# Kernel optimization log

Hardware: AMD Instinct MI355X
Metric: run time of the kernel (lower is better)

Reference implementation:

```python
import jax, jax.numpy as jnp
import numpy as np

N = 100000
E = 1600000
D_IN = 128
D_HID = 128
D_OUT = 64
NUM_LAYERS = 4


def setup_inputs() -> dict:
    key = jax.random.key(0)
    ks = jax.random.split(key, 12)
    features = jax.random.normal(ks[0], (N, D_IN), dtype=jnp.float32)
    edge_index = jax.random.randint(ks[1], (2, E), 0, N, dtype=jnp.int64)
    def glorot(k, shape):
        fan_in, fan_out = shape
        s = jnp.sqrt(6.0 / (fan_in + fan_out)).astype(jnp.float32)
        return jax.random.uniform(k, shape, jnp.float32, -s, s)
    W0 = glorot(ks[2], (D_IN, D_HID)); b0 = jnp.zeros((D_HID,), jnp.float32)
    W1 = glorot(ks[3], (D_HID, D_HID)); b1 = jnp.zeros((D_HID,), jnp.float32)
    W2 = glorot(ks[4], (D_HID, D_HID)); b2 = jnp.zeros((D_HID,), jnp.float32)
    W3 = glorot(ks[5], (D_HID, D_OUT)); b3 = jnp.zeros((D_OUT,), jnp.float32)
    return {"features": features, "edge_index": edge_index,
            "W0": W0, "b0": b0, "W1": W1, "b1": b1,
            "W2": W2, "b2": b2, "W3": W3, "b3": b3}


def _degree_norms(edge_index):
    src, dst = edge_index[0], edge_index[1]
    ones = jnp.ones((src.shape[0],), jnp.float32)
    out_deg = jax.ops.segment_sum(ones, src, num_segments=N)
    in_deg = jax.ops.segment_sum(ones, dst, num_segments=N)
    norm_src = jnp.where(out_deg > 0, jax.lax.rsqrt(jnp.maximum(out_deg, 1.0)), 0.0)
    norm_dst = jnp.where(in_deg > 0, jax.lax.rsqrt(jnp.maximum(in_deg, 1.0)), 0.0)
    return norm_src, norm_dst


def _graph_conv(x, W, b, src, dst, norm_src, norm_dst, act):
    # linear transform first (aggregation is linear, order-equivalent)
    h = x @ W                                   # [N, d_out]
    h = h * norm_src[:, None]                   # symmetric norm, src side
    msg = jnp.take(h, src, axis=0)              # gather  [E, d_out]
    agg = jax.ops.segment_sum(msg, dst, num_segments=N)  # scatter-add [N, d_out]
    agg = agg * norm_dst[:, None]               # symmetric norm, dst side
    agg = agg + b
    if act:
        agg = jnp.tanh(agg)
    return agg


def reference(features, edge_index, W0, b0, W1, b1, W2, b2, W3, b3):
    src, dst = edge_index[0], edge_index[1]
    norm_src, norm_dst = _degree_norms(edge_index)
    x = _graph_conv(features, W0, b0, src, dst, norm_src, norm_dst, act=True)
    x = _graph_conv(x, W1, b1, src, dst, norm_src, norm_dst, act=True)
    x = _graph_conv(x, W2, b2, src, dst, norm_src, norm_dst, act=True)
    x = _graph_conv(x, W3, b3, src, dst, norm_src, norm_dst, act=False)  # last layer: no activation
    return x
```

## Files before the change

kernel.cpp:

```cpp
#include <hip/hip_runtime.h>
#include <cmath>

typedef __attribute__((ext_vector_type(8))) short bf16x8;
typedef __attribute__((ext_vector_type(8))) _Float16 f16x8;
typedef __attribute__((ext_vector_type(4))) float f32x4;

__device__ inline unsigned short f2bf_rne(float f) {
    unsigned int u = __float_as_uint(f);
    unsigned int r = (u + 0x7FFFu + ((u >> 16) & 1u)) >> 16;
    return (unsigned short)r;
}
__device__ inline float bf2f(unsigned short h) {
    return __uint_as_float(((unsigned int)h) << 16);
}

__device__ inline float fast_tanh(float x) {
    float e = x * 2.8853900817779268f;
    e = fminf(fmaxf(e, -126.f), 126.f);
    float t = __builtin_amdgcn_exp2f(e);
    return (t - 1.0f) * __builtin_amdgcn_rcpf(t + 1.0f);
}


constexpr int CB = 256;

__global__ __launch_bounds__(256) void k_bucket_hist(const int* __restrict__ src,
                                                     const int* __restrict__ dst,
                                                     int* __restrict__ gH,
                                                     int E, int K, int scanN, int chunk) {
    extern __shared__ int lds[];
    int* hd = lds; int* hs = lds + K;
    for (int i = threadIdx.x; i < 2 * K; i += 256) lds[i] = 0;
    __syncthreads();
    int lo = blockIdx.x * chunk;
    int hi = lo + chunk; if (hi > E) hi = E;
    for (int i = lo + threadIdx.x; i < hi; i += 256) {
        atomicAdd(&hd[dst[i] >> 6], 1);
        atomicAdd(&hs[src[i] >> 6], 1);
    }
    __syncthreads();
    for (int k = threadIdx.x; k < K; k += 256) {
        gH[(size_t)k * CB + blockIdx.x] = hd[k];
        gH[(size_t)(scanN + k * CB) + blockIdx.x] = hs[k];
    }
}

__global__ __launch_bounds__(256) void k_bucket_scatter(const int* __restrict__ src,
                                                        const int* __restrict__ dst,
                                                        const int* __restrict__ gHS,
                                                        int* __restrict__ sortedAll,
                                                        int E, int K, int scanN, int chunk) {
    extern __shared__ int lds[];
    int* bd = lds; int* bs = lds + K;
    for (int k = threadIdx.x; k < K; k += 256) {
        bd[k] = gHS[(size_t)k * CB + blockIdx.x];
        bs[k] = gHS[(size_t)(scanN + k * CB) + blockIdx.x];
    }
    __syncthreads();
    int lo = blockIdx.x * chunk;
    int hi = lo + chunk; if (hi > E) hi = E;
    for (int i = lo + threadIdx.x; i < hi; i += 256) {
        int d = dst[i], s = src[i];
        int pd = atomicAdd(&bd[d >> 6], 1);
        sortedAll[pd] = ((d & 63) << 17) | s;
        int ps = atomicAdd(&bs[s >> 6], 1);
        sortedAll[ps] = s;
    }
}

__global__ __launch_bounds__(256) void k_fine(const int* __restrict__ sortedAll,
                                              const int* __restrict__ gHS,
                                              int* __restrict__ rowptr,
                                              int* __restrict__ colidx,
                                              float* __restrict__ nsrc,
                                              float* __restrict__ ndst,
                                              int E, int K, int scanN, int N) {
    __shared__ int cnt[64], excl[64], rank[64];
    int kb = blockIdx.x;
    bool isDst = kb < K;
    int k = isDst ? kb : kb - K;
    int bstart, bend;
    if (isDst) {
        bstart = gHS[(size_t)k * CB];
        bend = (k + 1 < K) ? gHS[(size_t)(k + 1) * CB] : E;
    } else {
        bstart = gHS[(size_t)(scanN + k * CB)];
        bend = (k + 1 < K) ? gHS[(size_t)(scanN + (k + 1) * CB)] : 2 * E;
    }
    if (threadIdx.x < 64) { cnt[threadIdx.x] = 0; rank[threadIdx.x] = 0; }
    __syncthreads();
    if (isDst) {
        for (int i = bstart + threadIdx.x; i < bend; i += 256)
            atomicAdd(&cnt[sortedAll[i] >> 17], 1);
    } else {
        for (int i = bstart + threadIdx.x; i < bend; i += 256)
            atomicAdd(&cnt[sortedAll[i] & 63], 1);
    }
    __syncthreads();
    if (isDst) {
        if (threadIdx.x == 0) {
            int r = 0;
            for (int j = 0; j < 64; j++) { excl[j] = r; r += cnt[j]; }
        }
        __syncthreads();
        int node0 = k << 6;
        if (threadIdx.x < 64) {
            int node = node0 + threadIdx.x;
            if (node < N) {
                rowptr[node] = bstart + excl[threadIdx.x];
                int c = cnt[threadIdx.x];
                ndst[node] = c > 0 ? rsqrtf((float)c) : 0.f;
            }
        }
        if (k == 0 && threadIdx.x == 0) rowptr[N] = E;
        for (int i = bstart + threadIdx.x; i < bend; i += 256) {
            int v = sortedAll[i];
            int n = v >> 17;
            int r = atomicAdd(&rank[n], 1);
            colidx[bstart + excl[n] + r] = v & 0x1FFFF;
        }
    } else {
        int node = (k << 6) + threadIdx.x;
        if (threadIdx.x < 64 && node < N) {
            int c = cnt[threadIdx.x];
            nsrc[node] = c > 0 ? rsqrtf((float)c) : 0.f;
        }
    }
}

__global__ void k_prepW_all(const float* __restrict__ W0, const float* __restrict__ W1,
                            const float* __restrict__ W2, const float* __restrict__ W3,
                            unsigned short* __restrict__ h0, unsigned short* __restrict__ l0,
                            unsigned short* __restrict__ h1, unsigned short* __restrict__ l1,
                            unsigned short* __restrict__ h2, unsigned short* __restrict__ l2,
                            unsigned short* __restrict__ h3, unsigned short* __restrict__ l3) {
    int i = blockIdx.x * 256 + threadIdx.x;
    const float* W; unsigned short* wh; unsigned short* wl; int N; int base; bool bf;
    if      (i < 16384) { W = W0; wh = h0; wl = l0; N = 128; base = i;         bf = true;  }
    else if (i < 32768) { W = W1; wh = h1; wl = l1; N = 128; base = i - 16384; bf = false; }
    else if (i < 49152) { W = W2; wh = h2; wl = l2; N = 128; base = i - 32768; bf = false; }
    else if (i < 57344) { W = W3; wh = h3; wl = l3; N = 64;  base = i - 49152; bf = false; }
    else return;
    int n = base >> 7, k = base & 127;
    float w = W[k * N + n];
    if (bf) {
        unsigned short hb = f2bf_rne(w);
        unsigned short lb = f2bf_rne(w - bf2f(hb));
        wh[base] = hb; wl[base] = lb;
    } else {
        union { _Float16 f; unsigned short u; } H, L;
        H.f = (_Float16)w;
        L.f = (_Float16)(w - (float)H.f);
        wh[base] = H.u; wl[base] = L.u;
    }
}


constexpr int SCAN_TILE = 2048;

__global__ __launch_bounds__(256) void k_scan_partial(const int* __restrict__ deg,
                                                      int* __restrict__ tilesum, int n) {
    __shared__ int red[256];
    int base = blockIdx.x * SCAN_TILE;
    int s = 0;
    for (int i = threadIdx.x; i < SCAN_TILE; i += 256) {
        int idx = base + i;
        if (idx < n) s += deg[idx];
    }
    red[threadIdx.x] = s;
    __syncthreads();
    for (int off = 128; off > 0; off >>= 1) {
        if (threadIdx.x < off) red[threadIdx.x] += red[threadIdx.x + off];
        __syncthreads();
    }
    if (threadIdx.x == 0) tilesum[blockIdx.x] = red[0];
}

__global__ void k_scan_tiles(int* __restrict__ tilesum, int* __restrict__ outArr,
                             int numTiles, int n) {
    if (threadIdx.x == 0 && blockIdx.x == 0) {
        int acc = 0;
        for (int i = 0; i < numTiles; i++) { int v = tilesum[i]; tilesum[i] = acc; acc += v; }
        outArr[n] = acc;
    }
}

__global__ __launch_bounds__(256) void k_scan_final(const int* __restrict__ deg,
                                                    const int* __restrict__ tilesum,
                                                    int* __restrict__ outArr, int n) {
    __shared__ int red[256];
    int base = blockIdx.x * SCAN_TILE;
    int lo = base + threadIdx.x * 8;
    int v[8]; int s = 0;
#pragma unroll
    for (int j = 0; j < 8; j++) {
        int idx = lo + j;
        v[j] = (idx < n) ? deg[idx] : 0;
        s += v[j];
    }
    red[threadIdx.x] = s;
    __syncthreads();
    for (int off = 1; off < 256; off <<= 1) {
        int x = red[threadIdx.x];
        int add = (threadIdx.x >= off) ? red[threadIdx.x - off] : 0;
        __syncthreads();
        red[threadIdx.x] = x + add;
        __syncthreads();
    }
    int excl = tilesum[blockIdx.x] + (threadIdx.x ? red[threadIdx.x - 1] : 0);
#pragma unroll
    for (int j = 0; j < 8; j++) {
        int idx = lo + j;
        if (idx < n) outArr[idx] = excl;
        excl += v[j];
    }
}


template <int DOUT, int SRC>
__global__ __launch_bounds__(256) void k_gemm_hyb(
        const float* __restrict__ xf, const _Float16* __restrict__ xq,
        const unsigned short* __restrict__ wth, const unsigned short* __restrict__ wtl,
        const float* __restrict__ nsrc, _Float16* __restrict__ h, int nrows) {
    constexpr int NT = DOUT / 16;
    constexpr int LDK = 72;
    __shared__ unsigned short Bh[DOUT * LDK], Bl[DOUT * LDK];

    int tid = threadIdx.x;
    int lane = tid & 63;
    int wv = tid >> 6;
    int quad = lane >> 4, l16 = lane & 15;
    int r0 = blockIdx.x * 64 + wv * 16;
    int rowA = r0 + l16; if (rowA >= nrows) rowA = nrows - 1;

    if (blockIdx.x == 0 && tid < DOUT / 8) {
        float4 z = {0.f, 0.f, 0.f, 0.f};
        *(float4*)((char*)h + ((size_t)nrows * DOUT + tid * 8) * 2) = z;
    }

    f32x4 acc[NT];
#pragma unroll
    for (int nt = 0; nt < NT; nt++) acc[nt] = (f32x4){0.f, 0.f, 0.f, 0.f};

    for (int kh = 0; kh < 2; kh++) {
        if (kh) __syncthreads();
        for (int i = tid; i < DOUT * 16; i += 256) {
            int n = i >> 4, kb = i & 15;
            int koff = kh * 64 + kb * 4;
            *(ushort4*)&Bh[n * LDK + kb * 4] = *(const ushort4*)&wth[n * 128 + koff];
            *(ushort4*)&Bl[n * LDK + kb * 4] = *(const ushort4*)&wtl[n * 128 + koff];
        }
        __syncthreads();

#pragma unroll
        for (int kq = 0; kq < 2; kq++) {
            int koA = kh * 64 + kq * 32 + quad * 8;
            int koB = kq * 32 + quad * 8;
            if (SRC == 0) {
                const float* xp = &xf[(size_t)rowA * 128 + koA];
                float4 x0 = *(const float4*)xp;
                float4 x1 = *(const float4*)(xp + 4);
                union { bf16x8 v; unsigned short u[8]; } H, L;
                float xs[8] = {x0.x, x0.y, x0.z, x0.w, x1.x, x1.y, x1.z, x1.w};
#pragma unroll
                for (int j = 0; j < 8; j++) {
                    H.u[j] = f2bf_rne(xs[j]);
                    L.u[j] = f2bf_rne(xs[j] - bf2f(H.u[j]));
                }
                bf16x8 ah = H.v, al = L.v;
#pragma unroll
                for (int nt = 0; nt < NT; nt++) {
                    int n = nt * 16 + l16;
                    bf16x8 bh = *(const bf16x8*)&Bh[n * LDK + koB];
                    bf16x8 bl = *(const bf16x8*)&Bl[n * LDK + koB];
                    acc[nt] = __builtin_amdgcn_mfma_f32_16x16x32_bf16(ah, bh, acc[nt], 0, 0, 0);
                    acc[nt] = __builtin_amdgcn_mfma_f32_16x16x32_bf16(ah, bl, acc[nt], 0, 0, 0);
                    acc[nt] = __builtin_amdgcn_mfma_f32_16x16x32_bf16(al, bh, acc[nt], 0, 0, 0);
                }
            } else {
                f16x8 aq = *(const f16x8*)&xq[(size_t)rowA * 128 + koA];
#pragma unroll
                for (int nt = 0; nt < NT; nt++) {
                    int n = nt * 16 + l16;
                    f16x8 bh = *(const f16x8*)&Bh[n * LDK + koB];
                    f16x8 bl = *(const f16x8*)&Bl[n * LDK + koB];
                    acc[nt] = __builtin_amdgcn_mfma_f32_16x16x32_f16(aq, bh, acc[nt], 0, 0, 0);
                    acc[nt] = __builtin_amdgcn_mfma_f32_16x16x32_f16(aq, bl, acc[nt], 0, 0, 0);
                }
            }
        }
    }

#pragma unroll
    for (int r = 0; r < 4; r++) {
        int row = r0 + quad * 4 + r;
        if (row < nrows) {
            float nm = nsrc[row];
#pragma unroll
            for (int nt = 0; nt < NT; nt++)
                h[(size_t)row * DOUT + nt * 16 + l16] = (_Float16)(acc[nt][r] * nm);
        }
    }
}


template <int D, int MODE>
__global__ __launch_bounds__(256) void k_aggregate(const _Float16* __restrict__ h,
                                                   const int* __restrict__ rowptr,
                                                   const int* __restrict__ colidx,
                                                   const float* __restrict__ ndst,
                                                   const float* __restrict__ bias,
                                                   float* __restrict__ out,
                                                   _Float16* __restrict__ oq,
                                                   int n) {
    constexpr int FB = D / 8;
    constexpr int GN = 64 / FB;
    constexpr int EU = 4;
    int wid  = (blockIdx.x * 256 + threadIdx.x) >> 6;
    int lane = threadIdx.x & 63;
    int fb = lane & (FB - 1);
    int g  = lane / FB;
    int waveCount = gridDim.x * 4;

    for (int nbase = wid * GN; nbase < n; nbase += waveCount * GN) {
        int node = nbase + g;
        bool vn = node < n;
        int beg = vn ? rowptr[node] : 0;
        int end = vn ? rowptr[node + 1] : 0;
        int m = end - beg;

        int mmax = m;
#pragma unroll
        for (int off = FB; off < 64; off <<= 1) {
            int t = __shfl_xor(mmax, off);
            mmax = mmax > t ? mmax : t;
        }

        float acc[8];
#pragma unroll
        for (int k = 0; k < 8; k++) acc[k] = 0.f;

        int cv = 0;
        for (int j0 = 0; j0 < mmax; j0 += EU) {
            if ((j0 & (FB - 1)) == 0) {
                int idx = beg + j0 + fb;
                cv = __builtin_nontemporal_load(&colidx[idx < end ? idx : 0]);
            }
            int s[EU];
#pragma unroll
            for (int u = 0; u < EU; u++) {
                int j = j0 + u;
                int sv = __shfl(cv, g * FB + (j & (FB - 1)));
                s[u] = j < m ? sv : n;
            }
            f16x8 v[EU];
#pragma unroll
            for (int u = 0; u < EU; u++)
                v[u] = *(const f16x8*)&h[(size_t)s[u] * D + fb * 8];
#pragma unroll
            for (int u = 0; u < EU; u++) {
#pragma unroll
                for (int k = 0; k < 8; k++)
                    acc[k] += (float)v[u][k];
            }
        }

        if (vn) {
            float nd = ndst[node];
            float bv[8];
            *(float4*)&bv[0] = ((const float4*)bias)[fb * 2];
            *(float4*)&bv[4] = ((const float4*)bias)[fb * 2 + 1];
            float vv[8];
#pragma unroll
            for (int k = 0; k < 8; k++) vv[k] = acc[k] * nd + bv[k];
            if (MODE == 1) {
                f16x8 q;
#pragma unroll
                for (int k = 0; k < 8; k++)
                    q[k] = (_Float16)fast_tanh(vv[k]);
                *(f16x8*)&oq[(size_t)node * D + fb * 8] = q;
            } else {
                *(float4*)&out[(size_t)node * D + fb * 8] = *(float4*)&vv[0];
                *(float4*)&out[(size_t)node * D + fb * 8 + 4] = *(float4*)&vv[4];
            }
        }
    }
}


extern "C" void kernel_launch(void* const* d_in, const int* in_sizes, int n_in,
                              void* d_out, int out_size, void* d_ws, size_t ws_size,
                              hipStream_t stream) {
    const float* features = (const float*)d_in[0];
    const int* edges      = (const int*)d_in[1];
    const float* W0 = (const float*)d_in[2]; const float* b0 = (const float*)d_in[3];
    const float* W1 = (const float*)d_in[4]; const float* b1 = (const float*)d_in[5];
    const float* W2 = (const float*)d_in[6]; const float* b2 = (const float*)d_in[7];
    const float* W3 = (const float*)d_in[8]; const float* b3 = (const float*)d_in[9];
    float* out = (float*)d_out;

    const int N = in_sizes[0] / 128;
    const int E = in_sizes[1] / 2;
    const int* src = edges;
    const int* dst = edges + E;
    const int K = (N + 63) >> 6;
    const int chunk = (E + CB - 1) / CB;
    const int scanN = K * CB;
    const int n2 = 2 * scanN;
    const int numTiles = (n2 + SCAN_TILE - 1) / SCAN_TILE;
    const size_t dynLds = (size_t)2 * K * sizeof(int);

    char* p = (char*)d_ws;
    _Float16* bufH         = (_Float16*)p;       p += (size_t)N * 128 * 4;
    _Float16* xq           = (_Float16*)p;       p += (size_t)(N + 1) * 128 * 2;
    char*     xspare       = p;                  p += (size_t)(N + 1) * 128 * 2;
    int*   rowptr = (int*)p;   p += (((size_t)(N + 1) * 4 + 15) / 16) * 16;
    int*   colidx = (int*)p;   p += (size_t)E * 4;
    float* nsrc   = (float*)p; p += (size_t)N * 4;
    float* ndst   = (float*)p; p += (size_t)N * 4;
    int*   tilesum= (int*)p;   p += (((size_t)(numTiles + 1) * 4 + 15) / 16) * 16;
    unsigned short* wt0h = (unsigned short*)p; p += 16384 * 2;
    unsigned short* wt0l = (unsigned short*)p; p += 16384 * 2;
    unsigned short* wt1h = (unsigned short*)p; p += 16384 * 2;
    unsigned short* wt1l = (unsigned short*)p; p += 16384 * 2;
    unsigned short* wt2h = (unsigned short*)p; p += 16384 * 2;
    unsigned short* wt2l = (unsigned short*)p; p += 16384 * 2;
    unsigned short* wt3h = (unsigned short*)p; p += 8192 * 2;
    unsigned short* wt3l = (unsigned short*)p; p += 8192 * 2;

    char* q = (char*)xq;
    int* sortedAll = (int*)q; q += (size_t)2 * E * 4;
    int* gH        = (int*)q; q += (size_t)n2 * 4;
    int* gHS       = (int*)q; q += (size_t)(n2 + 1) * 4;
    (void)xspare;

    k_prepW_all<<<224, 256, 0, stream>>>(W0, W1, W2, W3, wt0h, wt0l, wt1h, wt1l,
                                         wt2h, wt2l, wt3h, wt3l);
    k_bucket_hist<<<CB, 256, dynLds, stream>>>(src, dst, gH, E, K, scanN, chunk);
    k_scan_partial<<<numTiles, 256, 0, stream>>>(gH, tilesum, n2);
    k_scan_tiles<<<1, 64, 0, stream>>>(tilesum, gHS, numTiles, n2);
    k_scan_final<<<numTiles, 256, 0, stream>>>(gH, tilesum, gHS, n2);
    k_bucket_scatter<<<CB, 256, dynLds, stream>>>(src, dst, gHS, sortedAll, E, K, scanN, chunk);
    k_fine<<<2 * K, 256, 0, stream>>>(sortedAll, gHS, rowptr, colidx, nsrc, ndst, E, K, scanN, N);

    int gblk = (N + 63) / 64;
    int ablk128 = (N + 15) / 16;
    int ablk64  = (N + 31) / 32;
    k_gemm_hyb<128, 0><<<gblk, 256, 0, stream>>>(features, nullptr, wt0h, wt0l, nsrc, bufH, N);
    k_aggregate<128, 1><<<ablk128, 256, 0, stream>>>(bufH, rowptr, colidx, ndst, b0, nullptr, xq, N);
    k_gemm_hyb<128, 1><<<gblk, 256, 0, stream>>>(nullptr, xq, wt1h, wt1l, nsrc, bufH, N);
    k_aggregate<128, 1><<<ablk128, 256, 0, stream>>>(bufH, rowptr, colidx, ndst, b1, nullptr, xq, N);
    k_gemm_hyb<128, 1><<<gblk, 256, 0, stream>>>(nullptr, xq, wt2h, wt2l, nsrc, bufH, N);
    k_aggregate<128, 1><<<ablk128, 256, 0, stream>>>(bufH, rowptr, colidx, ndst, b2, nullptr, xq, N);
    k_gemm_hyb<64, 1><<<gblk, 256, 0, stream>>>(nullptr, xq, wt3h, wt3l, nsrc, bufH, N);
    k_aggregate<64, 0><<<ablk64, 256, 0, stream>>>(bufH, rowptr, colidx, ndst, b3, out, nullptr, N);
}
```

Before: 508.9 us.

## Compute out-degree with global atomics and tile multiple row blocks per GEMM wave

Out-degree is now counted with direct global atomics into a per-node array, zeroed in the weight-prep kernel. This drops the second half of the bucket sort, scan and fine pass that previously existed only to obtain source degrees. The GEMM kernel gains an RT template parameter so each wave handles two 16-row tiles, reusing the B fragments loaded from LDS across more MFMAs. Nontemporal loads and stores are added for activations. Global atomics on random source indices may contend, and the larger tiles raise register pressure.

```diff
diff --git a/kernel.cpp b/kernel.cpp
--- a/kernel.cpp
+++ b/kernel.cpp
@@ -27,35 +27,31 @@
 __global__ __launch_bounds__(256) void k_bucket_hist(const int* __restrict__ src,
                                                      const int* __restrict__ dst,
                                                      int* __restrict__ gH,
-                                                     int E, int K, int scanN, int chunk) {
+                                                     int* __restrict__ odeg,
+                                                     int E, int K, int chunk) {
     extern __shared__ int lds[];
-    int* hd = lds; int* hs = lds + K;
-    for (int i = threadIdx.x; i < 2 * K; i += 256) lds[i] = 0;
+    for (int i = threadIdx.x; i < K; i += 256) lds[i] = 0;
     __syncthreads();
     int lo = blockIdx.x * chunk;
     int hi = lo + chunk; if (hi > E) hi = E;
     for (int i = lo + threadIdx.x; i < hi; i += 256) {
-        atomicAdd(&hd[dst[i] >> 6], 1);
-        atomicAdd(&hs[src[i] >> 6], 1);
-    }
-    __syncthreads();
-    for (int k = threadIdx.x; k < K; k += 256) {
-        gH[(size_t)k * CB + blockIdx.x] = hd[k];
-        gH[(size_t)(scanN + k * CB) + blockIdx.x] = hs[k];
-    }
+        atomicAdd(&lds[dst[i] >> 6], 1);
+        atomicAdd(&odeg[src[i]], 1);
+    }
+    __syncthreads();
+    for (int k = threadIdx.x; k < K; k += 256)
+        gH[(size_t)k * CB + blockIdx.x] = lds[k];
 }
 
 __global__ __launch_bounds__(256) void k_bucket_scatter(const int* __restrict__ src,
                                                         const int* __restrict__ dst,
                                                         const int* __restrict__ gHS,
                                                         int* __restrict__ sortedAll,
-                                                        int E, int K, int scanN, int chunk) {
+                                                        int E, int K, int chunk) {
     extern __shared__ int lds[];
-    int* bd = lds; int* bs = lds + K;
-    for (int k = threadIdx.x; k < K; k += 256) {
+    int* bd = lds;
+    for (int k = threadIdx.x; k < K; k += 256)
         bd[k] = gHS[(size_t)k * CB + blockIdx.x];
-        bs[k] = gHS[(size_t)(scanN + k * CB) + blockIdx.x];
-    }
     __syncthreads();
     int lo = blockIdx.x * chunk;
     int hi = lo + chunk; if (hi > E) hi = E;
@@ -63,68 +59,48 @@
         int d = dst[i], s = src[i];
         int pd = atomicAdd(&bd[d >> 6], 1);
         sortedAll[pd] = ((d & 63) << 17) | s;
-        int ps = atomicAdd(&bs[s >> 6], 1);
-        sortedAll[ps] = s;
     }
 }
 
 __global__ __launch_bounds__(256) void k_fine(const int* __restrict__ sortedAll,
                                               const int* __restrict__ gHS,
+                                              const int* __restrict__ odeg,
                                               int* __restrict__ rowptr,
                                               int* __restrict__ colidx,
                                               float* __restrict__ nsrc,
                                               float* __restrict__ ndst,
-                                              int E, int K, int scanN, int N) {
+                                              int E, int K, int N) {
     __shared__ int cnt[64], excl[64], rank[64];
-    int kb = blockIdx.x;
-    bool isDst = kb < K;
-    int k = isDst ? kb : kb - K;
-    int bstart, bend;
-    if (isDst) {
-        bstart = gHS[(size_t)k * CB];
-        bend = (k + 1 < K) ? gHS[(size_t)(k + 1) * CB] : E;
-    } else {
-        bstart = gHS[(size_t)(scanN + k * CB)];
-        bend = (k + 1 < K) ? gHS[(size_t)(scanN + (k + 1) * CB)] : 2 * E;
-    }
+    int k = blockIdx.x;
+    int bstart = gHS[(size_t)k * CB];
+    int bend   = gHS[(size_t)(k + 1) * CB];
     if (threadIdx.x < 64) { cnt[threadIdx.x] = 0; rank[threadIdx.x] = 0; }
     __syncthreads();
-    if (isDst) {
-        for (int i = bstart + threadIdx.x; i < bend; i += 256)
-            atomicAdd(&cnt[sortedAll[i] >> 17], 1);
-    } else {
-        for (int i = bstart + threadIdx.x; i < bend; i += 256)
-            atomicAdd(&cnt[sortedAll[i] & 63], 1);
-    }
-    __syncthreads();
-    if (isDst) {
-        if (threadIdx.x == 0) {
-            int r = 0;
-            for (int j = 0; j < 64; j++) { excl[j] = r; r += cnt[j]; }
-        }
-        __syncthreads();
-        int node0 = k << 6;
-        if (threadIdx.x < 64) {
-            int node = node0 + threadIdx.x;
-            if (node < N) {
-                rowptr[node] = bstart + excl[threadIdx.x];
-                int c = cnt[threadIdx.x];
-                ndst[node] = c > 0 ? rsqrtf((float)c) : 0.f;
-            }
-        }
-        if (k == 0 && threadIdx.x == 0) rowptr[N] = E;
-        for (int i = bstart + threadIdx.x; i < bend; i += 256) {
-            int v = sortedAll[i];
-            int n = v >> 17;
-            int r = atomicAdd(&rank[n], 1);
-            colidx[bstart + excl[n] + r] = v & 0x1FFFF;
-        }
-    } else {
-        int node = (k << 6) + threadIdx.x;
-        if (threadIdx.x < 64 && node < N) {
+    for (int i = bstart + threadIdx.x; i < bend; i += 256)
+        atomicAdd(&cnt[sortedAll[i] >> 17], 1);
+    __syncthreads();
+    if (threadIdx.x == 0) {
+        int r = 0;
+        for (int j = 0; j < 64; j++) { excl[j] = r; r += cnt[j]; }
+    }
+    __syncthreads();
+    int node0 = k << 6;
+    if (threadIdx.x < 64) {
+        int node = node0 + threadIdx.x;
+        if (node < N) {
+            rowptr[node] = bstart + excl[threadIdx.x];
             int c = cnt[threadIdx.x];
-            nsrc[node] = c > 0 ? rsqrtf((float)c) : 0.f;
-        }
+            ndst[node] = c > 0 ? rsqrtf((float)c) : 0.f;
+            int od = odeg[node];
+            nsrc[node] = od > 0 ? rsqrtf((float)od) : 0.f;
+        }
+    }
+    if (k == 0 && threadIdx.x == 0) rowptr[N] = E;
+    for (int i = bstart + threadIdx.x; i < bend; i += 256) {
+        int v = sortedAll[i];
+        int nn = v >> 17;
+        int r = atomicAdd(&rank[nn], 1);
+        colidx[bstart + excl[nn] + r] = v & 0x1FFFF;
     }
 }
 
@@ -133,8 +109,10 @@
                             unsigned short* __restrict__ h0, unsigned short* __restrict__ l0,
                             unsigned short* __restrict__ h1, unsigned short* __restrict__ l1,
                             unsigned short* __restrict__ h2, unsigned short* __restrict__ l2,
-                            unsigned short* __restrict__ h3, unsigned short* __restrict__ l3) {
+                            unsigned short* __restrict__ h3, unsigned short* __restrict__ l3,
+                            int* __restrict__ odeg, int nodes) {
     int i = blockIdx.x * 256 + threadIdx.x;
+    if (i < nodes) odeg[i] = 0;
     const float* W; unsigned short* wh; unsigned short* wl; int N; int base; bool bf;
     if      (i < 16384) { W = W0; wh = h0; wl = l0; N = 128; base = i;         bf = true;  }
     else if (i < 32768) { W = W1; wh = h1; wl = l1; N = 128; base = i - 16384; bf = false; }
@@ -217,7 +195,7 @@
 }
 
 
-template <int DOUT, int SRC>
+template <int DOUT, int SRC, int RT>
 __global__ __launch_bounds__(256) void k_gemm_hyb(
         const float* __restrict__ xf, const _Float16* __restrict__ xq,
         const unsigned short* __restrict__ wth, const unsigned short* __restrict__ wtl,
@@ -230,17 +208,24 @@
     int lane = tid & 63;
     int wv = tid >> 6;
     int quad = lane >> 4, l16 = lane & 15;
-    int r0 = blockIdx.x * 64 + wv * 16;
-    int rowA = r0 + l16; if (rowA >= nrows) rowA = nrows - 1;
+    int r0 = blockIdx.x * (64 * RT) + wv * (16 * RT);
+    int rowA[RT];
+#pragma unroll
+    for (int t = 0; t < RT; t++) {
+        int r = r0 + t * 16 + l16;
+        rowA[t] = r < nrows ? r : nrows - 1;
+    }
 
     if (blockIdx.x == 0 && tid < DOUT / 8) {
-        float4 z = {0.f, 0.f, 0.f, 0.f};
-        *(float4*)((char*)h + ((size_t)nrows * DOUT + tid * 8) * 2) = z;
-    }
-
-    f32x4 acc[NT];
-#pragma unroll
-    for (int nt = 0; nt < NT; nt++) acc[nt] = (f32x4){0.f, 0.f, 0.f, 0.f};
+        f32x4 z = {0.f, 0.f, 0.f, 0.f};
+        *(f32x4*)((char*)h + ((size_t)nrows * DOUT + tid * 8) * 2) = z;
+    }
+
+    f32x4 acc[RT][NT];
+#pragma unroll
+    for (int t = 0; t < RT; t++)
+#pragma unroll
+        for (int nt = 0; nt < NT; nt++) acc[t][nt] = (f32x4){0.f, 0.f, 0.f, 0.f};
 
     for (int kh = 0; kh < 2; kh++) {
         if (kh) __syncthreads();
@@ -257,50 +242,65 @@
             int koA = kh * 64 + kq * 32 + quad * 8;
             int koB = kq * 32 + quad * 8;
             if (SRC == 0) {
-                const float* xp = &xf[(size_t)rowA * 128 + koA];
-                float4 x0 = *(const float4*)xp;
-                float4 x1 = *(const float4*)(xp + 4);
-                union { bf16x8 v; unsigned short u[8]; } H, L;
-                float xs[8] = {x0.x, x0.y, x0.z, x0.w, x1.x, x1.y, x1.z, x1.w};
-#pragma unroll
-                for (int j = 0; j < 8; j++) {
-                    H.u[j] = f2bf_rne(xs[j]);
-                    L.u[j] = f2bf_rne(xs[j] - bf2f(H.u[j]));
+                bf16x8 ah[RT], al[RT];
+#pragma unroll
+                for (int t = 0; t < RT; t++) {
+                    const float* xp = &xf[(size_t)rowA[t] * 128 + koA];
+                    f32x4 x0 = __builtin_nontemporal_load((const f32x4*)xp);
+                    f32x4 x1 = __builtin_nontemporal_load((const f32x4*)(xp + 4));
+                    union { bf16x8 v; unsigned short u[8]; } H, L;
+                    float xs[8] = {x0[0], x0[1], x0[2], x0[3], x1[0], x1[1], x1[2], x1[3]};
+#pragma unroll
+                    for (int j = 0; j < 8; j++) {
+                        H.u[j] = f2bf_rne(xs[j]);
+                        L.u[j] = f2bf_rne(xs[j] - bf2f(H.u[j]));
+                    }
+                    ah[t] = H.v; al[t] = L.v;
                 }
-                bf16x8 ah = H.v, al = L.v;
 #pragma unroll
                 for (int nt = 0; nt < NT; nt++) {
                     int n = nt * 16 + l16;
                     bf16x8 bh = *(const bf16x8*)&Bh[n * LDK + koB];
                     bf16x8 bl = *(const bf16x8*)&Bl[n * LDK + koB];
-                    acc[nt] = __builtin_amdgcn_mfma_f32_16x16x32_bf16(ah, bh, acc[nt], 0, 0, 0);
-                    acc[nt] = __builtin_amdgcn_mfma_f32_16x16x32_bf16(ah, bl, acc[nt], 0, 0, 0);
-                    acc[nt] = __builtin_amdgcn_mfma_f32_16x16x32_bf16(al, bh, acc[nt], 0, 0, 0);
+#pragma unroll
+                    for (int t = 0; t < RT; t++) {
+                        acc[t][nt] = __builtin_amdgcn_mfma_f32_16x16x32_bf16(ah[t], bh, acc[t][nt], 0, 0, 0);
+                        acc[t][nt] = __builtin_amdgcn_mfma_f32_16x16x32_bf16(ah[t], bl, acc[t][nt], 0, 0, 0);
+                        acc[t][nt] = __builtin_amdgcn_mfma_f32_16x16x32_bf16(al[t], bh, acc[t][nt], 0, 0, 0);
+                    }
                 }
             } else {
-                f16x8 aq = *(const f16x8*)&xq[(size_t)rowA * 128 + koA];
+                f16x8 aq[RT];
+#pragma unroll
+                for (int t = 0; t < RT; t++)
+                    aq[t] = __builtin_nontemporal_load((const f16x8*)&xq[(size_t)rowA[t] * 128 + koA]);
 #pragma unroll
                 for (int nt = 0; nt < NT; nt++) {
                     int n = nt * 16 + l16;
                     f16x8 bh = *(const f16x8*)&Bh[n * LDK + koB];
                     f16x8 bl = *(const f16x8*)&Bl[n * LDK + koB];
-                    acc[nt] = __builtin_amdgcn_mfma_f32_16x16x32_f16(aq, bh, acc[nt], 0, 0, 0);
-                    acc[nt] = __builtin_amdgcn_mfma_f32_16x16x32_f16(aq, bl, acc[nt], 0, 0, 0);
+#pragma unroll
+                    for (int t = 0; t < RT; t++) {
+                        acc[t][nt] = __builtin_amdgcn_mfma_f32_16x16x32_f16(aq[t], bh, acc[t][nt], 0, 0, 0);
+                        acc[t][nt] = __builtin_amdgcn_mfma_f32_16x16x32_f16(aq[t], bl, acc[t][nt], 0, 0, 0);
+                    }
                 }
             }
         }
     }
 
 #pragma unroll
-    for (int r = 0; r < 4; r++) {
-        int row = r0 + quad * 4 + r;
-        if (row < nrows) {
-            float nm = nsrc[row];
-#pragma unroll
-            for (int nt = 0; nt < NT; nt++)
-                h[(size_t)row * DOUT + nt * 16 + l16] = (_Float16)(acc[nt][r] * nm);
-        }
-    }
+    for (int t = 0; t < RT; t++)
+#pragma unroll
+        for (int r = 0; r < 4; r++) {
+            int row = r0 + t * 16 + quad * 4 + r;
+            if (row < nrows) {
+                float nm = nsrc[row];
+#pragma unroll
+                for (int nt = 0; nt < NT; nt++)
+                    h[(size_t)row * DOUT + nt * 16 + l16] = (_Float16)(acc[t][nt][r] * nm);
+            }
+        }
 }
 
 
@@ -378,10 +378,10 @@
 #pragma unroll
                 for (int k = 0; k < 8; k++)
                     q[k] = (_Float16)fast_tanh(vv[k]);
-                *(f16x8*)&oq[(size_t)node * D + fb * 8] = q;
+                __builtin_nontemporal_store(q, (f16x8*)&oq[(size_t)node * D + fb * 8]);
             } else {
-                *(float4*)&out[(size_t)node * D + fb * 8] = *(float4*)&vv[0];
-                *(float4*)&out[(size_t)node * D + fb * 8 + 4] = *(float4*)&vv[4];
+                __builtin_nontemporal_store(*(f32x4*)&vv[0], (f32x4*)&out[(size_t)node * D + fb * 8]);
+                __builtin_nontemporal_store(*(f32x4*)&vv[4], (f32x4*)&out[(size_t)node * D + fb * 8 + 4]);
             }
         }
     }
@@ -406,18 +406,17 @@
     const int K = (N + 63) >> 6;
     const int chunk = (E + CB - 1) / CB;
     const int scanN = K * CB;
-    const int n2 = 2 * scanN;
-    const int numTiles = (n2 + SCAN_TILE - 1) / SCAN_TILE;
-    const size_t dynLds = (size_t)2 * K * sizeof(int);
+    const int numTiles = (scanN + SCAN_TILE - 1) / SCAN_TILE;
+    const size_t dynLds = (size_t)K * sizeof(int);
 
     char* p = (char*)d_ws;
     _Float16* bufH         = (_Float16*)p;       p += (size_t)N * 128 * 4;
     _Float16* xq           = (_Float16*)p;       p += (size_t)(N + 1) * 128 * 2;
-    char*     xspare       = p;                  p += (size_t)(N + 1) * 128 * 2;
     int*   rowptr = (int*)p;   p += (((size_t)(N + 1) * 4 + 15) / 16) * 16;
     int*   colidx = (int*)p;   p += (size_t)E * 4;
     float* nsrc   = (float*)p; p += (size_t)N * 4;
     float* ndst   = (float*)p; p += (size_t)N * 4;
+    int*   odeg   = (int*)p;   p += (size_t)N * 4;
     int*   tilesum= (int*)p;   p += (((size_t)(numTiles + 1) * 4 + 15) / 16) * 16;
     unsigned short* wt0h = (unsigned short*)p; p += 16384 * 2;
     unsigned short* wt0l = (unsigned short*)p; p += 16384 * 2;
@@ -429,29 +428,30 @@
     unsigned short* wt3l = (unsigned short*)p; p += 8192 * 2;
 
     char* q = (char*)xq;
-    int* sortedAll = (int*)q; q += (size_t)2 * E * 4;
-    int* gH        = (int*)q; q += (size_t)n2 * 4;
-    int* gHS       = (int*)q; q += (size_t)(n2 + 1) * 4;
-    (void)xspare;
-
-    k_prepW_all<<<224, 256, 0, stream>>>(W0, W1, W2, W3, wt0h, wt0l, wt1h, wt1l,
-                                         wt2h, wt2l, wt3h, wt3l);
-    k_bucket_hist<<<CB, 256, dynLds, stream>>>(src, dst, gH, E, K, scanN, chunk);
-    k_scan_partial<<<numTiles, 256, 0, stream>>>(gH, tilesum, n2);
-    k_scan_tiles<<<1, 64, 0, stream>>>(tilesum, gHS, numTiles, n2);
-    k_scan_final<<<numTiles, 256, 0, stream>>>(gH, tilesum, gHS, n2);
-    k_bucket_scatter<<<CB, 256, dynLds, stream>>>(src, dst, gHS, sortedAll, E, K, scanN, chunk);
-    k_fine<<<2 * K, 256, 0, stream>>>(sortedAll, gHS, rowptr, colidx, nsrc, ndst, E, K, scanN, N);
-
-    int gblk = (N + 63) / 64;
+    int* sortedAll = (int*)q; q += (size_t)E * 4;
+    int* gH        = (int*)q; q += (size_t)scanN * 4;
+    int* gHS       = (int*)q; q += (size_t)(scanN + 1) * 4;
+
+    int prepBlocks = (N + 255) / 256; if (prepBlocks < 224) prepBlocks = 224;
+    k_prepW_all<<<prepBlocks, 256, 0, stream>>>(W0, W1, W2, W3, wt0h, wt0l, wt1h, wt1l,
+                                                wt2h, wt2l, wt3h, wt3l, odeg, N);
+    k_bucket_hist<<<CB, 256, dynLds, stream>>>(src, dst, gH, odeg, E, K, chunk);
+    k_scan_partial<<<numTiles, 256, 0, stream>>>(gH, tilesum, scanN);
+    k_scan_tiles<<<1, 64, 0, stream>>>(tilesum, gHS, numTiles, scanN);
+    k_scan_final<<<numTiles, 256, 0, stream>>>(gH, tilesum, gHS, scanN);
+    k_bucket_scatter<<<CB, 256, dynLds, stream>>>(src, dst, gHS, sortedAll, E, K, chunk);
+    k_fine<<<K, 256, 0, stream>>>(sortedAll, gHS, odeg, rowptr, colidx, nsrc, ndst, E, K, N);
+
+    int gblk1 = (N + 63) / 64;
+    int gblk2 = (N + 127) / 128;
     int ablk128 = (N + 15) / 16;
     int ablk64  = (N + 31) / 32;
-    k_gemm_hyb<128, 0><<<gblk, 256, 0, stream>>>(features, nullptr, wt0h, wt0l, nsrc, bufH, N);
+    k_gemm_hyb<128, 0, 1><<<gblk1, 256, 0, stream>>>(features, nullptr, wt0h, wt0l, nsrc, bufH, N);
     k_aggregate<128, 1><<<ablk128, 256, 0, stream>>>(bufH, rowptr, colidx, ndst, b0, nullptr, xq, N);
-    k_gemm_hyb<128, 1><<<gblk, 256, 0, stream>>>(nullptr, xq, wt1h, wt1l, nsrc, bufH, N);
+    k_gemm_hyb<128, 1, 2><<<gblk2, 256, 0, stream>>>(nullptr, xq, wt1h, wt1l, nsrc, bufH, N);
     k_aggregate<128, 1><<<ablk128, 256, 0, stream>>>(bufH, rowptr, colidx, ndst, b1, nullptr, xq, N);
-    k_gemm_hyb<128, 1><<<gblk, 256, 0, stream>>>(nullptr, xq, wt2h, wt2l, nsrc, bufH, N);
+    k_gemm_hyb<128, 1, 2><<<gblk2, 256, 0, stream>>>(nullptr, xq, wt2h, wt2l, nsrc, bufH, N);
     k_aggregate<128, 1><<<ablk128, 256, 0, stream>>>(bufH, rowptr, colidx, ndst, b2, nullptr, xq, N);
-    k_gemm_hyb<64, 1><<<gblk, 256, 0, stream>>>(nullptr, xq, wt3h, wt3l, nsrc, bufH, N);
+    k_gemm_hyb<64, 1, 2><<<gblk2, 256, 0, stream>>>(nullptr, xq, wt3h, wt3l, nsrc, bufH, N);
     k_aggregate<64, 0><<<ablk64, 256, 0, stream>>>(bufH, rowptr, colidx, ndst, b3, out, nullptr, N);
 }
```

Result: slower. 533.2 us (+4.8%).
